# Performance work log

Measured on AMD Instinct MI355X. Metric: run time of the kernel, lower is better.

Reference implementation:

```python
import jax, jax.numpy as jnp
import numpy as np

B, N, D, A, R, E = 4, 50000, 128, 128, 200, 600000  # batch, entities, hidden dim, attn dim, relations, edges


def setup_inputs() -> dict:
    key = jax.random.key(0)
    ks = jax.random.split(key, 18)
    sD = 1.0 / np.sqrt(D)
    sA = 1.0 / np.sqrt(A)
    id_bat = jax.random.randint(ks[0], (E,), 0, B)
    id_sub = id_bat * N + jax.random.randint(ks[1], (E,), 0, N)
    id_rel = jax.random.randint(ks[2], (E,), 0, R)
    id_obj = id_bat * N + jax.random.randint(ks[3], (E,), 0, N)
    edges = jnp.stack([id_bat, id_sub, id_rel, id_obj], axis=1)
    return {
        "query": jax.random.normal(ks[4], (B, D), jnp.float32),
        "q_sub": jax.random.randint(ks[5], (B,), 0, N),
        "q_rel": jax.random.randint(ks[6], (B,), 0, R),
        "hidden": jax.random.normal(ks[7], (B, N, D), jnp.float32),
        "edges": edges,
        "nodes": jax.random.randint(ks[8], (B, 2), 0, N),
        "Ws_attn_w": jax.random.normal(ks[9], (A, D), jnp.float32) * sD,
        "Wr_attn_w": jax.random.normal(ks[10], (A, D), jnp.float32) * sD,
        "Wqr_attn_w": jax.random.normal(ks[11], (A, D), jnp.float32) * sD,
        "Wqr_attn_b": jax.random.normal(ks[12], (A,), jnp.float32) * sD,
        "W_attn_w": jax.random.normal(ks[13], (1, A), jnp.float32) * sA,
        "rela_embed": jax.random.normal(ks[14], (R, D), jnp.float32) * sD,
        "mlp1_w": jax.random.normal(ks[15], (D, D), jnp.float32) * sD,
        "mlp1_b": jnp.zeros((D,), jnp.float32),
        "mlp2_w": jax.random.normal(ks[16], (D, D), jnp.float32) * sD,
        "mlp2_b": jnp.zeros((D,), jnp.float32),
    }


def reference(query, q_sub, q_rel, hidden, edges, nodes,
              Ws_attn_w, Wr_attn_w, Wqr_attn_w, Wqr_attn_b, W_attn_w,
              rela_embed, mlp1_w, mlp1_b, mlp2_w, mlp2_b):
    b, n, d = hidden.shape
    id_bat, id_sub, id_rel, id_obj = edges[:, 0], edges[:, 1], edges[:, 2], edges[:, 3]
    all_ent = hidden.reshape(b * n, d)                       # [B*N, D]
    mh = all_ent[id_sub]                                     # [E, D] gather heads
    mr = rela_embed[id_rel]                                  # [E, D] gather relations
    mq = query[id_bat]                                       # [E, D] gather queries
    mess = mh * mr                                           # distmult message
    # attention MLP: sigmoid(W_attn @ relu(Ws h + Wr r + Wqr q + b))
    h_attn = jax.nn.relu(mh @ Ws_attn_w.T + mr @ Wr_attn_w.T + mq @ Wqr_attn_w.T + Wqr_attn_b)
    alpha = jax.nn.sigmoid(h_attn @ W_attn_w.T)              # [E, 1]
    message = mess * alpha
    # scatter-sum aggregate over destination nodes
    agg = jax.ops.segment_sum(message, id_obj, num_segments=b * n)   # [B*N, D]
    # mask of nodes that received at least one message (== torch.unique(id_obj))
    deg = jax.ops.segment_sum(jnp.ones((id_obj.shape[0],), jnp.float32), id_obj, num_segments=b * n)
    recv = deg > 0                                           # [B*N]
    # per-row MLP: Linear -> Linear -> ReLU (mlp_num=2, no activation between)
    h = jax.nn.relu((agg @ mlp1_w.T + mlp1_b) @ mlp2_w.T + mlp2_b)
    new_hidden = jnp.where(recv[:, None], h, 0.0).reshape(b, n, d)
    return new_hidden
```

## Files before the change

### kernel.cpp

```cpp
#include <hip/hip_runtime.h>

typedef unsigned int u32;
typedef unsigned short u16;
typedef __attribute__((ext_vector_type(8))) short bf16x8;
typedef __attribute__((ext_vector_type(4))) float f32x4;

#define Bb 4
#define Nn 50000
#define Dd 128
#define Rr 200
#define BN (Bb*Nn)
#define MAXDEG 32
#define LDW 136

__device__ __forceinline__ float bfs(u16 u) { return __uint_as_float(((u32)u) << 16); }
__device__ __forceinline__ float bflo(u32 u) { return __uint_as_float(u << 16); }
__device__ __forceinline__ float bfhi(u32 u) { return __uint_as_float(u & 0xffff0000u); }
__device__ __forceinline__ u16 f2bf(float f) {
    u32 x = __float_as_uint(f);
    return (u16)((x + 0x7fffu + ((x >> 16) & 1u)) >> 16);
}
template<bool BF>
__device__ __forceinline__ float ld1(const void* p, int i) {
    if (BF) return bfs(((const u16*)p)[i]);
    else    return ((const float*)p)[i];
}

__global__ void k_probe(const u32* __restrict__ q, int* __restrict__ flag) {
    int t = threadIdx.x;
    u32 w = q[t];
    int e = (int)((w >> 7) & 0xffu);
    bool plaus = (e >= 100 && e <= 150);
    unsigned long long m = __ballot(plaus);
    if (t == 0) flag[0] = (__popcll(m) >= 56) ? 1 : 0;
}

__global__ __launch_bounds__(256) void k_wprep(
    const void* Ws, const void* w1, const void* w2,
    const void* b1, const void* b2, const void* wattn, const void* rela,
    u16* WsH, u16* WsL, u16* w1H, u16* w1L, u16* w2H, u16* w2L,
    float* b1f, float* b2f, float* wattnf, float* relaf, const int* flag) {
    bool bf = (*flag != 0);
    int i = blockIdx.x * 256 + threadIdx.x;
    if (i < 16384) {
        float x = bf ? bfs(((const u16*)Ws)[i]) : ((const float*)Ws)[i];
        u16 h = f2bf(x); WsH[i] = h; WsL[i] = f2bf(x - bfs(h));
    } else if (i < 32768) {
        int j = i - 16384;
        float x = bf ? bfs(((const u16*)w1)[j]) : ((const float*)w1)[j];
        u16 h = f2bf(x); w1H[j] = h; w1L[j] = f2bf(x - bfs(h));
    } else if (i < 49152) {
        int j = i - 32768;
        float x = bf ? bfs(((const u16*)w2)[j]) : ((const float*)w2)[j];
        u16 h = f2bf(x); w2H[j] = h; w2L[j] = f2bf(x - bfs(h));
    } else if (i < 49152 + 128) {
        int j = i - 49152;
        b1f[j] = bf ? bfs(((const u16*)b1)[j]) : ((const float*)b1)[j];
    } else if (i < 49152 + 256) {
        int j = i - 49152 - 128;
        b2f[j] = bf ? bfs(((const u16*)b2)[j]) : ((const float*)b2)[j];
    } else if (i < 49152 + 384) {
        int j = i - 49152 - 256;
        wattnf[j] = bf ? bfs(((const u16*)wattn)[j]) : ((const float*)wattn)[j];
    } else if (i < 49152 + 384 + 25600) {
        int j = i - 49152 - 384;
        relaf[j] = bf ? bfs(((const u16*)rela)[j]) : ((const float*)rela)[j];
    }
}

template<bool BF>
__device__ __forceinline__ float dotrow1(const void* W, int row, const float* s) {
    float acc = 0.f;
    if (BF) {
        const uint4* wv = (const uint4*)((const u16*)W + row * Dd);
#pragma unroll
        for (int k = 0; k < 16; k++) {
            uint4 u = wv[k];
            acc += bflo(u.x)*s[k*8+0] + bfhi(u.x)*s[k*8+1]
                 + bflo(u.y)*s[k*8+2] + bfhi(u.y)*s[k*8+3]
                 + bflo(u.z)*s[k*8+4] + bfhi(u.z)*s[k*8+5]
                 + bflo(u.w)*s[k*8+6] + bfhi(u.w)*s[k*8+7];
        }
    } else {
        const float4* wv = (const float4*)((const float*)W + row * Dd);
#pragma unroll
        for (int k = 0; k < 32; k++) {
            float4 u = wv[k];
            acc += u.x*s[4*k] + u.y*s[4*k+1] + u.z*s[4*k+2] + u.w*s[4*k+3];
        }
    }
    return acc;
}
template<bool BF>
__device__ void k_wrq_body(const void* Wr, const void* Wqr, const void* bias,
                           const void* rela, const void* query, float* wrq) {
    int br = blockIdx.x;
    int b = br / Rr, r = br % Rr;
    int a = threadIdx.x;
    __shared__ float s[2 * Dd];
    s[a]      = ld1<BF>(rela,  r * Dd + a);
    s[Dd + a] = ld1<BF>(query, b * Dd + a);
    __syncthreads();
    wrq[br * Dd + a] = ld1<BF>(bias, a) + dotrow1<BF>(Wr, a, s) + dotrow1<BF>(Wqr, a, s + Dd);
}
__global__ __launch_bounds__(128) void k_wrq(const void* Wr, const void* Wqr, const void* bias,
                                             const void* rela, const void* query, float* wrq,
                                             const int* flag) {
    if (*flag) k_wrq_body<true>(Wr, Wqr, bias, rela, query, wrq);
    else       k_wrq_body<false>(Wr, Wqr, bias, rela, query, wrq);
}

__device__ __forceinline__ void stage_f32(const float* src, u16* Ah, u16* Al, int t) {
#pragma unroll
    for (int it = 0; it < 8; it++) {
        int idx = it * 256 + t;
        int row = idx >> 5, c4 = (idx & 31) << 2;
        float4 v = ((const float4*)src)[idx];
        u16 h0 = f2bf(v.x), h1 = f2bf(v.y), h2 = f2bf(v.z), h3 = f2bf(v.w);
        ushort4 hv; hv.x = h0; hv.y = h1; hv.z = h2; hv.w = h3;
        ushort4 lv; lv.x = f2bf(v.x - bfs(h0)); lv.y = f2bf(v.y - bfs(h1));
                    lv.z = f2bf(v.z - bfs(h2)); lv.w = f2bf(v.w - bfs(h3));
        *(ushort4*)(Ah + row * LDW + c4) = hv;
        *(ushort4*)(Al + row * LDW + c4) = lv;
    }
}
__device__ __forceinline__ void stage_bf(const u16* src, u16* Ah, u16* Al, int t) {
#pragma unroll
    for (int it = 0; it < 4; it++) {
        int idx = it * 256 + t;
        int row = idx >> 4, c8 = (idx & 15) << 3;
        uint4 v = ((const uint4*)src)[idx];
        *(uint4*)(Ah + row * LDW + c8) = v;
        uint4 z; z.x = 0; z.y = 0; z.z = 0; z.w = 0;
        *(uint4*)(Al + row * LDW + c8) = z;
    }
}

template<bool BF>
__device__ void k_hs_body(const void* hidden, const u16* WsH, const u16* WsL, u16* hs) {
    __shared__ u16 Ah[64 * LDW], Al[64 * LDW];
    int t = threadIdx.x, n0 = blockIdx.x * 64;
    if (BF) stage_bf((const u16*)hidden + (size_t)n0 * Dd, Ah, Al, t);
    else    stage_f32((const float*)hidden + (size_t)n0 * Dd, Ah, Al, t);
    __syncthreads();
    int w = t >> 6, lane = t & 63, m16 = lane & 15, quad = lane >> 4;
    const u16* rowh = Ah + (w * 16 + m16) * LDW + quad * 8;
    const u16* rowl = Al + (w * 16 + m16) * LDW + quad * 8;
    bf16x8 ah[4], al[4];
#pragma unroll
    for (int ks = 0; ks < 4; ks++) {
        ah[ks] = *(const bf16x8*)(rowh + ks * 32);
        al[ks] = *(const bf16x8*)(rowl + ks * 32);
    }
#pragma unroll
    for (int nt = 0; nt < 8; nt++) {
        int n = nt * 16 + m16;
        f32x4 acc = {0.f, 0.f, 0.f, 0.f};
#pragma unroll
        for (int ks = 0; ks < 4; ks++) {
            bf16x8 bh = *(const bf16x8*)(WsH + n * Dd + ks * 32 + quad * 8);
            bf16x8 bl = *(const bf16x8*)(WsL + n * Dd + ks * 32 + quad * 8);
            acc = __builtin_amdgcn_mfma_f32_16x16x32_bf16(ah[ks], bh, acc, 0, 0, 0);
            acc = __builtin_amdgcn_mfma_f32_16x16x32_bf16(al[ks], bh, acc, 0, 0, 0);
            acc = __builtin_amdgcn_mfma_f32_16x16x32_bf16(ah[ks], bl, acc, 0, 0, 0);
        }
#pragma unroll
        for (int r = 0; r < 4; r++) {
            int node = n0 + w * 16 + quad * 4 + r;
            hs[(size_t)node * Dd + n] = f2bf(acc[r]);
        }
    }
}
__global__ __launch_bounds__(256) void k_hs(const void* hidden, const u16* WsH, const u16* WsL,
                                            u16* hs, const int* flag) {
    if (*flag) k_hs_body<true>(hidden, WsH, WsL, hs);
    else       k_hs_body<false>(hidden, WsH, WsL, hs);
}

__global__ __launch_bounds__(256) void k_scatter(const int* __restrict__ edges,
                                                 u32* __restrict__ slots, u32* __restrict__ eslot,
                                                 int* __restrict__ deg, int nE) {
    int i = blockIdx.x * 256 + threadIdx.x;
    if (i >= nE) return;
    int bat = edges[4*i], sub = edges[4*i+1], rel = edges[4*i+2], obj = edges[4*i+3];
    int pos = atomicAdd(&deg[obj], 1);
    if (pos < MAXDEG) {
        u32 sl = (u32)obj * MAXDEG + pos;
        slots[sl] = (u32)sub | ((u32)rel << 18) | ((u32)bat << 26);
        eslot[i] = sl;
    } else eslot[i] = 0xFFFFFFFFu;
}

__global__ __launch_bounds__(256) void k_alpha(const int4* __restrict__ edges,
                                               const u16* __restrict__ hs,
                                               const float* __restrict__ wrq,
                                               const float* __restrict__ wattnf,
                                               const u32* __restrict__ eslot,
                                               float* __restrict__ alphaslot, int nE) {
    int wid = ((blockIdx.x * 256) + threadIdx.x) >> 6;
    int lane = threadIdx.x & 63;
    if (wid >= nE) return;
    int4 e = edges[wid];
    int bat = e.x, sub = e.y, rel = e.z;
    u32 hp = ((const u32*)hs)[sub * 64 + lane];
    float2 wq = ((const float2*)wrq)[(bat * Rr + rel) * 64 + lane];
    float2 wa = ((const float2*)wattnf)[lane];
    float h0 = fmaxf(bflo(hp) + wq.x, 0.f);
    float h1 = fmaxf(bfhi(hp) + wq.y, 0.f);
    float p = h0 * wa.x + h1 * wa.y;
#pragma unroll
    for (int m = 32; m >= 1; m >>= 1) p += __shfl_xor(p, m);
    if (lane == 0) {
        u32 sl = eslot[wid];
        if (sl != 0xFFFFFFFFu) alphaslot[sl] = 1.f / (1.f + __expf(-p));
    }
}

template<bool BF>
__device__ void k_agg_body(const u32* __restrict__ slots, const float* __restrict__ alphaslot,
                           const int* __restrict__ deg, const void* __restrict__ hidden,
                           const float* __restrict__ relaf, float* __restrict__ agg) {
    int wid = ((blockIdx.x * 256) + threadIdx.x) >> 6;
    int lane = threadIdx.x & 63;
    if (wid >= BN) return;
    int d = deg[wid]; if (d > MAXDEG) d = MAXDEG;
    float a0 = 0.f, a1 = 0.f;
    for (int e = 0; e < d; e++) {
        u32 rec = slots[wid * MAXDEG + e];
        float alpha = alphaslot[wid * MAXDEG + e];
        int sub = rec & 0x3FFFF, rel = (rec >> 18) & 0xFF;
        float mh0, mh1;
        if (BF) { u32 mh = ((const u32*)hidden)[sub * 64 + lane]; mh0 = bflo(mh); mh1 = bfhi(mh); }
        else    { float2 mh = ((const float2*)hidden)[sub * 64 + lane]; mh0 = mh.x; mh1 = mh.y; }
        float2 mr = ((const float2*)relaf)[rel * 64 + lane];
        a0 += mh0 * mr.x * alpha;
        a1 += mh1 * mr.y * alpha;
    }
    float2 v; v.x = a0; v.y = a1;
    ((float2*)agg)[(size_t)wid * 64 + lane] = v;
}
__global__ __launch_bounds__(256) void k_agg(const u32* slots, const float* alphaslot,
                                             const int* deg, const void* hidden,
                                             const float* relaf, float* agg, const int* flag) {
    if (*flag) k_agg_body<true>(slots, alphaslot, deg, hidden, relaf, agg);
    else       k_agg_body<false>(slots, alphaslot, deg, hidden, relaf, agg);
}

template<bool BF>
__device__ void k_mlp_body(const float* agg, const int* deg,
                           const u16* w1H, const u16* w1L, const u16* w2H, const u16* w2L,
                           const float* b1f, const float* b2f, void* out) {
    __shared__ u16 Ah[64 * LDW], Al[64 * LDW];
    int t = threadIdx.x, n0 = blockIdx.x * 64;
    stage_f32(agg + (size_t)n0 * Dd, Ah, Al, t);
    __syncthreads();
    int w = t >> 6, lane = t & 63, m16 = lane & 15, quad = lane >> 4;
    u16* rowh = Ah + (w * 16 + m16) * LDW + quad * 8;
    u16* rowl = Al + (w * 16 + m16) * LDW + quad * 8;
    bf16x8 ah[4], al[4];
#pragma unroll
    for (int ks = 0; ks < 4; ks++) {
        ah[ks] = *(const bf16x8*)(rowh + ks * 32);
        al[ks] = *(const bf16x8*)(rowl + ks * 32);
    }
#pragma unroll
    for (int nt = 0; nt < 8; nt++) {
        int n = nt * 16 + m16;
        f32x4 acc = {0.f, 0.f, 0.f, 0.f};
#pragma unroll
        for (int ks = 0; ks < 4; ks++) {
            bf16x8 bh = *(const bf16x8*)(w1H + n * Dd + ks * 32 + quad * 8);
            bf16x8 bl = *(const bf16x8*)(w1L + n * Dd + ks * 32 + quad * 8);
            acc = __builtin_amdgcn_mfma_f32_16x16x32_bf16(ah[ks], bh, acc, 0, 0, 0);
            acc = __builtin_amdgcn_mfma_f32_16x16x32_bf16(al[ks], bh, acc, 0, 0, 0);
            acc = __builtin_amdgcn_mfma_f32_16x16x32_bf16(ah[ks], bl, acc, 0, 0, 0);
        }
        float bv = b1f[n];
#pragma unroll
        for (int r = 0; r < 4; r++) {
            float v = acc[r] + bv;
            int row = w * 16 + quad * 4 + r;
            u16 h = f2bf(v);
            Ah[row * LDW + n] = h;
            Al[row * LDW + n] = f2bf(v - bfs(h));
        }
    }
    bf16x8 mh[4], ml[4];
#pragma unroll
    for (int ks = 0; ks < 4; ks++) {
        mh[ks] = *(const bf16x8*)(rowh + ks * 32);
        ml[ks] = *(const bf16x8*)(rowl + ks * 32);
    }
    int dg[4];
#pragma unroll
    for (int r = 0; r < 4; r++) dg[r] = deg[n0 + w * 16 + quad * 4 + r];
#pragma unroll
    for (int nt = 0; nt < 8; nt++) {
        int n = nt * 16 + m16;
        f32x4 acc = {0.f, 0.f, 0.f, 0.f};
#pragma unroll
        for (int ks = 0; ks < 4; ks++) {
            bf16x8 bh = *(const bf16x8*)(w2H + n * Dd + ks * 32 + quad * 8);
            bf16x8 bl = *(const bf16x8*)(w2L + n * Dd + ks * 32 + quad * 8);
            acc = __builtin_amdgcn_mfma_f32_16x16x32_bf16(mh[ks], bh, acc, 0, 0, 0);
            acc = __builtin_amdgcn_mfma_f32_16x16x32_bf16(ml[ks], bh, acc, 0, 0, 0);
            acc = __builtin_amdgcn_mfma_f32_16x16x32_bf16(mh[ks], bl, acc, 0, 0, 0);
        }
        float bv = b2f[n];
#pragma unroll
        for (int r = 0; r < 4; r++) {
            float v = fmaxf(acc[r] + bv, 0.f);
            if (dg[r] == 0) v = 0.f;
            size_t o = (size_t)(n0 + w * 16 + quad * 4 + r) * Dd + n;
            if (BF) ((u16*)out)[o] = f2bf(v);
            else    ((float*)out)[o] = v;
        }
    }
}
__global__ __launch_bounds__(256) void k_mlp(const float* agg, const int* deg,
                                             const u16* w1H, const u16* w1L,
                                             const u16* w2H, const u16* w2L,
                                             const float* b1f, const float* b2f,
                                             void* out, const int* flag) {
    if (*flag) k_mlp_body<true>(agg, deg, w1H, w1L, w2H, w2L, b1f, b2f, out);
    else       k_mlp_body<false>(agg, deg, w1H, w1L, w2H, w2L, b1f, b2f, out);
}

extern "C" void kernel_launch(void* const* d_in, const int* in_sizes, int n_in,
                              void* d_out, int out_size, void* d_ws, size_t ws_size,
                              hipStream_t stream) {
    const void* query  = d_in[0];
    const void* hidden = d_in[3];
    const int*  edges  = (const int*)d_in[4];
    const void* Ws     = d_in[6];
    const void* Wr     = d_in[7];
    const void* Wqr    = d_in[8];
    const void* Wqrb   = d_in[9];
    const void* Wattn  = d_in[10];
    const void* rela   = d_in[11];
    const void* w1     = d_in[12];
    const void* b1     = d_in[13];
    const void* w2     = d_in[14];
    const void* b2     = d_in[15];

    char* ws = (char*)d_ws;
    float* agg    = (float*)ws;
    u16*   hs     = (u16*)ws;
    float* wrq    = (float*)(ws +  51200000);
    u32*   eslot  = (u32*) (ws +  51609600);
    u32*   slots  = (u32*) (ws + 102400000);
    float* alphas = (float*)(ws + 128000000);
    int*   deg    = (int*) (ws + 153600000);
    u16*   WsH    = (u16*) (ws + 154400000);
    u16*   WsL    = (u16*) (ws + 154432768);
    u16*   w1H    = (u16*) (ws + 154465536);
    u16*   w1L    = (u16*) (ws + 154498304);
    u16*   w2H    = (u16*) (ws + 154531072);
    u16*   w2L    = (u16*) (ws + 154563840);
    float* b1f    = (float*)(ws + 154596608);
    float* b2f    = (float*)(ws + 154597120);
    float* wattnf = (float*)(ws + 154597632);
    float* relaf  = (float*)(ws + 154598144);
    int*   flag   = (int*) (ws + 154700544);

    int nE = in_sizes[4] / 4;

    k_probe<<<1, 64, 0, stream>>>((const u32*)query, flag);
    hipMemsetAsync(deg, 0, (size_t)BN * 4, stream);
    k_wprep<<<294, 256, 0, stream>>>(Ws, w1, w2, b1, b2, Wattn, rela,
                                     WsH, WsL, w1H, w1L, w2H, w2L,
                                     b1f, b2f, wattnf, relaf, flag);
    k_wrq<<<Bb * Rr, 128, 0, stream>>>(Wr, Wqr, Wqrb, rela, query, wrq, flag);
    k_hs<<<BN / 64, 256, 0, stream>>>(hidden, WsH, WsL, hs, flag);
    k_scatter<<<(nE + 255) / 256, 256, 0, stream>>>(edges, slots, eslot, deg, nE);
    k_alpha<<<(nE + 3) / 4, 256, 0, stream>>>((const int4*)edges, hs, wrq, wattnf,
                                              eslot, alphas, nE);
    k_agg<<<(BN + 3) / 4, 256, 0, stream>>>(slots, alphas, deg, hidden, relaf, agg, flag);
    k_mlp<<<BN / 64, 256, 0, stream>>>(agg, deg, w1H, w1L, w2H, w2L, b1f, b2f, d_out, flag);
}
```

Measured before the change: 826.7 us.

## Fuse alpha, aggregation and MLP into one per-wave kernel

```diff
diff --git a/kernel.cpp b/kernel.cpp
--- a/kernel.cpp
+++ b/kernel.cpp
@@ -12,6 +12,7 @@
 #define BN (Bb*Nn)
 #define MAXDEG 32
 #define LDW 136
+#define SLAB 4352
 
 __device__ __forceinline__ float bfs(u16 u) { return __uint_as_float(((u32)u) << 16); }
 __device__ __forceinline__ float bflo(u32 u) { return __uint_as_float(u << 16); }
@@ -110,47 +111,46 @@
     else       k_wrq_body<false>(Wr, Wqr, bias, rela, query, wrq);
 }
 
-__device__ __forceinline__ void stage_f32(const float* src, u16* Ah, u16* Al, int t) {
-#pragma unroll
-    for (int it = 0; it < 8; it++) {
-        int idx = it * 256 + t;
-        int row = idx >> 5, c4 = (idx & 31) << 2;
-        float4 v = ((const float4*)src)[idx];
-        u16 h0 = f2bf(v.x), h1 = f2bf(v.y), h2 = f2bf(v.z), h3 = f2bf(v.w);
-        ushort4 hv; hv.x = h0; hv.y = h1; hv.z = h2; hv.w = h3;
-        ushort4 lv; lv.x = f2bf(v.x - bfs(h0)); lv.y = f2bf(v.y - bfs(h1));
-                    lv.z = f2bf(v.z - bfs(h2)); lv.w = f2bf(v.w - bfs(h3));
-        *(ushort4*)(Ah + row * LDW + c4) = hv;
-        *(ushort4*)(Al + row * LDW + c4) = lv;
-    }
-}
-__device__ __forceinline__ void stage_bf(const u16* src, u16* Ah, u16* Al, int t) {
-#pragma unroll
-    for (int it = 0; it < 4; it++) {
-        int idx = it * 256 + t;
-        int row = idx >> 4, c8 = (idx & 15) << 3;
-        uint4 v = ((const uint4*)src)[idx];
-        *(uint4*)(Ah + row * LDW + c8) = v;
-        uint4 z; z.x = 0; z.y = 0; z.z = 0; z.w = 0;
-        *(uint4*)(Al + row * LDW + c8) = z;
-    }
-}
-
-template<bool BF>
-__device__ void k_hs_body(const void* hidden, const u16* WsH, const u16* WsL, u16* hs) {
-    __shared__ u16 Ah[64 * LDW], Al[64 * LDW];
-    int t = threadIdx.x, n0 = blockIdx.x * 64;
-    if (BF) stage_bf((const u16*)hidden + (size_t)n0 * Dd, Ah, Al, t);
-    else    stage_f32((const float*)hidden + (size_t)n0 * Dd, Ah, Al, t);
-    __syncthreads();
-    int w = t >> 6, lane = t & 63, m16 = lane & 15, quad = lane >> 4;
-    const u16* rowh = Ah + (w * 16 + m16) * LDW + quad * 8;
-    const u16* rowl = Al + (w * 16 + m16) * LDW + quad * 8;
+template<bool BF>
+__device__ void hs_body(const void* hidden, const u16* WsH, const u16* WsL, u16* hs) {
+    __shared__ u16 SL[4][SLAB];
+    int t = threadIdx.x, w = t >> 6, lane = t & 63;
+    int m16 = lane & 15, quad = lane >> 4;
+    int base = blockIdx.x * 64 + w * 16;
+    u16* Smh = SL[w];
+    u16* Sml = SL[w] + 16 * LDW;
+
+    if (BF) {
+        const u16* src = (const u16*)hidden + (size_t)base * Dd;
+#pragma unroll
+        for (int j = 0; j < 4; j++) {
+            int flat = j * 64 + lane;
+            int row = flat >> 4, c8 = (flat & 15) * 8;
+            uint4 v = ((const uint4*)src)[flat];
+            *(uint4*)(Smh + row * LDW + c8) = v;
+        }
+    } else {
+        const float* src = (const float*)hidden + (size_t)base * Dd;
+#pragma unroll
+        for (int j = 0; j < 8; j++) {
+            int flat = j * 64 + lane;
+            int row = flat >> 5, c4 = (flat & 31) * 4;
+            float4 v = ((const float4*)src)[flat];
+            u16 h0 = f2bf(v.x), h1 = f2bf(v.y), h2 = f2bf(v.z), h3 = f2bf(v.w);
+            ushort4 hv; hv.x = h0; hv.y = h1; hv.z = h2; hv.w = h3;
+            ushort4 lv; lv.x = f2bf(v.x - bfs(h0)); lv.y = f2bf(v.y - bfs(h1));
+                        lv.z = f2bf(v.z - bfs(h2)); lv.w = f2bf(v.w - bfs(h3));
+            *(ushort4*)(Smh + row * LDW + c4) = hv;
+            *(ushort4*)(Sml + row * LDW + c4) = lv;
+        }
+    }
+    const u16* ph = Smh + m16 * LDW + quad * 8;
+    const u16* pl = Sml + m16 * LDW + quad * 8;
     bf16x8 ah[4], al[4];
 #pragma unroll
     for (int ks = 0; ks < 4; ks++) {
-        ah[ks] = *(const bf16x8*)(rowh + ks * 32);
-        al[ks] = *(const bf16x8*)(rowl + ks * 32);
+        ah[ks] = *(const bf16x8*)(ph + ks * 32);
+        if (!BF) al[ks] = *(const bf16x8*)(pl + ks * 32);
     }
 #pragma unroll
     for (int nt = 0; nt < 8; nt++) {
@@ -159,109 +159,102 @@
 #pragma unroll
         for (int ks = 0; ks < 4; ks++) {
             bf16x8 bh = *(const bf16x8*)(WsH + n * Dd + ks * 32 + quad * 8);
-            bf16x8 bl = *(const bf16x8*)(WsL + n * Dd + ks * 32 + quad * 8);
             acc = __builtin_amdgcn_mfma_f32_16x16x32_bf16(ah[ks], bh, acc, 0, 0, 0);
-            acc = __builtin_amdgcn_mfma_f32_16x16x32_bf16(al[ks], bh, acc, 0, 0, 0);
-            acc = __builtin_amdgcn_mfma_f32_16x16x32_bf16(ah[ks], bl, acc, 0, 0, 0);
-        }
-#pragma unroll
-        for (int r = 0; r < 4; r++) {
-            int node = n0 + w * 16 + quad * 4 + r;
-            hs[(size_t)node * Dd + n] = f2bf(acc[r]);
-        }
-    }
-}
-__global__ __launch_bounds__(256) void k_hs(const void* hidden, const u16* WsH, const u16* WsL,
-                                            u16* hs, const int* flag) {
-    if (*flag) k_hs_body<true>(hidden, WsH, WsL, hs);
-    else       k_hs_body<false>(hidden, WsH, WsL, hs);
+            if (!BF) {
+                bf16x8 bl = *(const bf16x8*)(WsL + n * Dd + ks * 32 + quad * 8);
+                acc = __builtin_amdgcn_mfma_f32_16x16x32_bf16(al[ks], bh, acc, 0, 0, 0);
+                acc = __builtin_amdgcn_mfma_f32_16x16x32_bf16(ah[ks], bl, acc, 0, 0, 0);
+            }
+        }
+#pragma unroll
+        for (int r = 0; r < 4; r++)
+            hs[(size_t)(base + quad * 4 + r) * Dd + n] = f2bf(acc[r]);
+    }
+}
+__global__ __launch_bounds__(256, 4) void k_hs(const void* hidden, const u16* WsH,
+                                               const u16* WsL, u16* hs, const int* flag) {
+    if (*flag) hs_body<true>(hidden, WsH, WsL, hs);
+    else       hs_body<false>(hidden, WsH, WsL, hs);
 }
 
 __global__ __launch_bounds__(256) void k_scatter(const int* __restrict__ edges,
-                                                 u32* __restrict__ slots, u32* __restrict__ eslot,
+                                                 u32* __restrict__ slots,
                                                  int* __restrict__ deg, int nE) {
     int i = blockIdx.x * 256 + threadIdx.x;
     if (i >= nE) return;
     int bat = edges[4*i], sub = edges[4*i+1], rel = edges[4*i+2], obj = edges[4*i+3];
     int pos = atomicAdd(&deg[obj], 1);
-    if (pos < MAXDEG) {
-        u32 sl = (u32)obj * MAXDEG + pos;
-        slots[sl] = (u32)sub | ((u32)rel << 18) | ((u32)bat << 26);
-        eslot[i] = sl;
-    } else eslot[i] = 0xFFFFFFFFu;
-}
-
-__global__ __launch_bounds__(256) void k_alpha(const int4* __restrict__ edges,
-                                               const u16* __restrict__ hs,
-                                               const float* __restrict__ wrq,
-                                               const float* __restrict__ wattnf,
-                                               const u32* __restrict__ eslot,
-                                               float* __restrict__ alphaslot, int nE) {
-    int wid = ((blockIdx.x * 256) + threadIdx.x) >> 6;
-    int lane = threadIdx.x & 63;
-    if (wid >= nE) return;
-    int4 e = edges[wid];
-    int bat = e.x, sub = e.y, rel = e.z;
+    if (pos < MAXDEG)
+        slots[obj * MAXDEG + pos] = (u32)sub | ((u32)rel << 18) | ((u32)bat << 26);
+}
+
+template<bool BF>
+__device__ __forceinline__ void edge_msg(u32 rec, int lane, float2 wa,
+                                         const u16* hs, const float* wrq,
+                                         const void* hidden, const float* relaf,
+                                         float& a0, float& a1) {
+    int sub = rec & 0x3FFFF, rel = (rec >> 18) & 0xFF, bat = (int)(rec >> 26);
     u32 hp = ((const u32*)hs)[sub * 64 + lane];
     float2 wq = ((const float2*)wrq)[(bat * Rr + rel) * 64 + lane];
-    float2 wa = ((const float2*)wattnf)[lane];
+    float mh0, mh1;
+    if (BF) { u32 mh = ((const u32*)hidden)[sub * 64 + lane]; mh0 = bflo(mh); mh1 = bfhi(mh); }
+    else    { float2 mh = ((const float2*)hidden)[sub * 64 + lane]; mh0 = mh.x; mh1 = mh.y; }
+    float2 mr = ((const float2*)relaf)[rel * 64 + lane];
     float h0 = fmaxf(bflo(hp) + wq.x, 0.f);
     float h1 = fmaxf(bfhi(hp) + wq.y, 0.f);
     float p = h0 * wa.x + h1 * wa.y;
 #pragma unroll
     for (int m = 32; m >= 1; m >>= 1) p += __shfl_xor(p, m);
-    if (lane == 0) {
-        u32 sl = eslot[wid];
-        if (sl != 0xFFFFFFFFu) alphaslot[sl] = 1.f / (1.f + __expf(-p));
-    }
-}
-
-template<bool BF>
-__device__ void k_agg_body(const u32* __restrict__ slots, const float* __restrict__ alphaslot,
-                           const int* __restrict__ deg, const void* __restrict__ hidden,
-                           const float* __restrict__ relaf, float* __restrict__ agg) {
-    int wid = ((blockIdx.x * 256) + threadIdx.x) >> 6;
-    int lane = threadIdx.x & 63;
-    if (wid >= BN) return;
-    int d = deg[wid]; if (d > MAXDEG) d = MAXDEG;
-    float a0 = 0.f, a1 = 0.f;
-    for (int e = 0; e < d; e++) {
-        u32 rec = slots[wid * MAXDEG + e];
-        float alpha = alphaslot[wid * MAXDEG + e];
-        int sub = rec & 0x3FFFF, rel = (rec >> 18) & 0xFF;
-        float mh0, mh1;
-        if (BF) { u32 mh = ((const u32*)hidden)[sub * 64 + lane]; mh0 = bflo(mh); mh1 = bfhi(mh); }
-        else    { float2 mh = ((const float2*)hidden)[sub * 64 + lane]; mh0 = mh.x; mh1 = mh.y; }
-        float2 mr = ((const float2*)relaf)[rel * 64 + lane];
-        a0 += mh0 * mr.x * alpha;
-        a1 += mh1 * mr.y * alpha;
-    }
-    float2 v; v.x = a0; v.y = a1;
-    ((float2*)agg)[(size_t)wid * 64 + lane] = v;
-}
-__global__ __launch_bounds__(256) void k_agg(const u32* slots, const float* alphaslot,
-                                             const int* deg, const void* hidden,
-                                             const float* relaf, float* agg, const int* flag) {
-    if (*flag) k_agg_body<true>(slots, alphaslot, deg, hidden, relaf, agg);
-    else       k_agg_body<false>(slots, alphaslot, deg, hidden, relaf, agg);
-}
-
-template<bool BF>
-__device__ void k_mlp_body(const float* agg, const int* deg,
+    float alpha = 1.f / (1.f + __expf(-p));
+    a0 += mh0 * mr.x * alpha;
+    a1 += mh1 * mr.y * alpha;
+}
+
+template<bool BF>
+__device__ void fused_body(const u32* __restrict__ slots, const int* __restrict__ deg,
+                           const u16* __restrict__ hs, const float* __restrict__ wrq,
+                           const float* __restrict__ wattnf,
+                           const void* __restrict__ hidden, const float* __restrict__ relaf,
                            const u16* w1H, const u16* w1L, const u16* w2H, const u16* w2L,
                            const float* b1f, const float* b2f, void* out) {
-    __shared__ u16 Ah[64 * LDW], Al[64 * LDW];
-    int t = threadIdx.x, n0 = blockIdx.x * 64;
-    stage_f32(agg + (size_t)n0 * Dd, Ah, Al, t);
-    __syncthreads();
-    int w = t >> 6, lane = t & 63, m16 = lane & 15, quad = lane >> 4;
-    u16* rowh = Ah + (w * 16 + m16) * LDW + quad * 8;
-    u16* rowl = Al + (w * 16 + m16) * LDW + quad * 8;
+    __shared__ u16 SL[4][SLAB];
+    int t = threadIdx.x, w = t >> 6, lane = t & 63;
+    int m16 = lane & 15, quad = lane >> 4;
+    int base = blockIdx.x * 64 + w * 16;
+    u16* Smh = SL[w];
+    u16* Sml = SL[w] + 16 * LDW;
+    float2 wa = ((const float2*)wattnf)[lane];
+
+    for (int i = 0; i < 16; i++) {
+        int node = base + i;
+        int d = deg[node]; if (d > MAXDEG) d = MAXDEG;
+        float a0 = 0.f, a1 = 0.f;
+        float c0 = 0.f, c1 = 0.f;
+        int e = 0;
+        for (; e + 1 < d; e += 2) {
+            u32 r0 = slots[node * MAXDEG + e];
+            u32 r1 = slots[node * MAXDEG + e + 1];
+            edge_msg<BF>(r0, lane, wa, hs, wrq, hidden, relaf, a0, a1);
+            edge_msg<BF>(r1, lane, wa, hs, wrq, hidden, relaf, c0, c1);
+        }
+        if (e < d) {
+            u32 r0 = slots[node * MAXDEG + e];
+            edge_msg<BF>(r0, lane, wa, hs, wrq, hidden, relaf, a0, a1);
+        }
+        a0 += c0; a1 += c1;
+        u16 h0 = f2bf(a0); u16 l0 = f2bf(a0 - bfs(h0));
+        u16 h1 = f2bf(a1); u16 l1 = f2bf(a1 - bfs(h1));
+        *(u32*)(Smh + i * LDW + 2 * lane) = (u32)h0 | ((u32)h1 << 16);
+        *(u32*)(Sml + i * LDW + 2 * lane) = (u32)l0 | ((u32)l1 << 16);
+    }
+
+    const u16* ph = Smh + m16 * LDW + quad * 8;
+    const u16* pl = Sml + m16 * LDW + quad * 8;
     bf16x8 ah[4], al[4];
 #pragma unroll
     for (int ks = 0; ks < 4; ks++) {
-        ah[ks] = *(const bf16x8*)(rowh + ks * 32);
-        al[ks] = *(const bf16x8*)(rowl + ks * 32);
+        ah[ks] = *(const bf16x8*)(ph + ks * 32);
+        al[ks] = *(const bf16x8*)(pl + ks * 32);
     }
 #pragma unroll
     for (int nt = 0; nt < 8; nt++) {
@@ -270,30 +263,33 @@
 #pragma unroll
         for (int ks = 0; ks < 4; ks++) {
             bf16x8 bh = *(const bf16x8*)(w1H + n * Dd + ks * 32 + quad * 8);
-            bf16x8 bl = *(const bf16x8*)(w1L + n * Dd + ks * 32 + quad * 8);
             acc = __builtin_amdgcn_mfma_f32_16x16x32_bf16(ah[ks], bh, acc, 0, 0, 0);
             acc = __builtin_amdgcn_mfma_f32_16x16x32_bf16(al[ks], bh, acc, 0, 0, 0);
-            acc = __builtin_amdgcn_mfma_f32_16x16x32_bf16(ah[ks], bl, acc, 0, 0, 0);
+            if (!BF) {
+                bf16x8 bl = *(const bf16x8*)(w1L + n * Dd + ks * 32 + quad * 8);
+                acc = __builtin_amdgcn_mfma_f32_16x16x32_bf16(ah[ks], bl, acc, 0, 0, 0);
+            }
         }
         float bv = b1f[n];
 #pragma unroll
         for (int r = 0; r < 4; r++) {
             float v = acc[r] + bv;
-            int row = w * 16 + quad * 4 + r;
+            int row = quad * 4 + r;
             u16 h = f2bf(v);
-            Ah[row * LDW + n] = h;
-            Al[row * LDW + n] = f2bf(v - bfs(h));
-        }
-    }
+            Smh[row * LDW + n] = h;
+            Sml[row * LDW + n] = f2bf(v - bfs(h));
+        }
+    }
+
     bf16x8 mh[4], ml[4];
 #pragma unroll
     for (int ks = 0; ks < 4; ks++) {
-        mh[ks] = *(const bf16x8*)(rowh + ks * 32);
-        ml[ks] = *(const bf16x8*)(rowl + ks * 32);
+        mh[ks] = *(const bf16x8*)(ph + ks * 32);
+        ml[ks] = *(const bf16x8*)(pl + ks * 32);
     }
     int dg[4];
 #pragma unroll
-    for (int r = 0; r < 4; r++) dg[r] = deg[n0 + w * 16 + quad * 4 + r];
+    for (int r = 0; r < 4; r++) dg[r] = deg[base + quad * 4 + r];
 #pragma unroll
     for (int nt = 0; nt < 8; nt++) {
         int n = nt * 16 + m16;
@@ -301,29 +297,36 @@
 #pragma unroll
         for (int ks = 0; ks < 4; ks++) {
             bf16x8 bh = *(const bf16x8*)(w2H + n * Dd + ks * 32 + quad * 8);
-            bf16x8 bl = *(const bf16x8*)(w2L + n * Dd + ks * 32 + quad * 8);
             acc = __builtin_amdgcn_mfma_f32_16x16x32_bf16(mh[ks], bh, acc, 0, 0, 0);
             acc = __builtin_amdgcn_mfma_f32_16x16x32_bf16(ml[ks], bh, acc, 0, 0, 0);
-            acc = __builtin_amdgcn_mfma_f32_16x16x32_bf16(mh[ks], bl, acc, 0, 0, 0);
+            if (!BF) {
+                bf16x8 bl = *(const bf16x8*)(w2L + n * Dd + ks * 32 + quad * 8);
+                acc = __builtin_amdgcn_mfma_f32_16x16x32_bf16(mh[ks], bl, acc, 0, 0, 0);
+            }
         }
         float bv = b2f[n];
 #pragma unroll
         for (int r = 0; r < 4; r++) {
             float v = fmaxf(acc[r] + bv, 0.f);
             if (dg[r] == 0) v = 0.f;
-            size_t o = (size_t)(n0 + w * 16 + quad * 4 + r) * Dd + n;
+            size_t o = (size_t)(base + quad * 4 + r) * Dd + n;
             if (BF) ((u16*)out)[o] = f2bf(v);
             else    ((float*)out)[o] = v;
         }
     }
 }
-__global__ __launch_bounds__(256) void k_mlp(const float* agg, const int* deg,
-                                             const u16* w1H, const u16* w1L,
-                                             const u16* w2H, const u16* w2L,
-                                             const float* b1f, const float* b2f,
-                                             void* out, const int* flag) {
-    if (*flag) k_mlp_body<true>(agg, deg, w1H, w1L, w2H, w2L, b1f, b2f, out);
-    else       k_mlp_body<false>(agg, deg, w1H, w1L, w2H, w2L, b1f, b2f, out);
+__global__ __launch_bounds__(256, 4) void k_fused(const u32* slots, const int* deg,
+                                                  const u16* hs, const float* wrq,
+                                                  const float* wattnf, const void* hidden,
+                                                  const float* relaf,
+                                                  const u16* w1H, const u16* w1L,
+                                                  const u16* w2H, const u16* w2L,
+                                                  const float* b1f, const float* b2f,
+                                                  void* out, const int* flag) {
+    if (*flag) fused_body<true>(slots, deg, hs, wrq, wattnf, hidden, relaf,
+                                w1H, w1L, w2H, w2L, b1f, b2f, out);
+    else       fused_body<false>(slots, deg, hs, wrq, wattnf, hidden, relaf,
+                                 w1H, w1L, w2H, w2L, b1f, b2f, out);
 }
 
 extern "C" void kernel_launch(void* const* d_in, const int* in_sizes, int n_in,
@@ -344,24 +347,21 @@
     const void* b2     = d_in[15];
 
     char* ws = (char*)d_ws;
-    float* agg    = (float*)ws;
     u16*   hs     = (u16*)ws;
     float* wrq    = (float*)(ws +  51200000);
-    u32*   eslot  = (u32*) (ws +  51609600);
-    u32*   slots  = (u32*) (ws + 102400000);
-    float* alphas = (float*)(ws + 128000000);
-    int*   deg    = (int*) (ws + 153600000);
-    u16*   WsH    = (u16*) (ws + 154400000);
-    u16*   WsL    = (u16*) (ws + 154432768);
-    u16*   w1H    = (u16*) (ws + 154465536);
-    u16*   w1L    = (u16*) (ws + 154498304);
-    u16*   w2H    = (u16*) (ws + 154531072);
-    u16*   w2L    = (u16*) (ws + 154563840);
-    float* b1f    = (float*)(ws + 154596608);
-    float* b2f    = (float*)(ws + 154597120);
-    float* wattnf = (float*)(ws + 154597632);
-    float* relaf  = (float*)(ws + 154598144);
-    int*   flag   = (int*) (ws + 154700544);
+    u32*   slots  = (u32*) (ws +  51609600);
+    int*   deg    = (int*) (ws +  77209600);
+    u16*   WsH    = (u16*) (ws +  78009600);
+    u16*   WsL    = (u16*) (ws +  78042368);
+    u16*   w1H    = (u16*) (ws +  78075136);
+    u16*   w1L    = (u16*) (ws +  78107904);
+    u16*   w2H    = (u16*) (ws +  78140672);
+    u16*   w2L    = (u16*) (ws +  78173440);
+    float* b1f    = (float*)(ws +  78206208);
+    float* b2f    = (float*)(ws +  78206720);
+    float* wattnf = (float*)(ws +  78207232);
+    float* relaf  = (float*)(ws +  78207744);
+    int*   flag   = (int*) (ws +  78310144);
 
     int nE = in_sizes[4] / 4;
 
@@ -372,9 +372,7 @@
                                      b1f, b2f, wattnf, relaf, flag);
     k_wrq<<<Bb * Rr, 128, 0, stream>>>(Wr, Wqr, Wqrb, rela, query, wrq, flag);
     k_hs<<<BN / 64, 256, 0, stream>>>(hidden, WsH, WsL, hs, flag);
-    k_scatter<<<(nE + 255) / 256, 256, 0, stream>>>(edges, slots, eslot, deg, nE);
-    k_alpha<<<(nE + 3) / 4, 256, 0, stream>>>((const int4*)edges, hs, wrq, wattnf,
-                                              eslot, alphas, nE);
-    k_agg<<<(BN + 3) / 4, 256, 0, stream>>>(slots, alphas, deg, hidden, relaf, agg, flag);
-    k_mlp<<<BN / 64, 256, 0, stream>>>(agg, deg, w1H, w1L, w2H, w2L, b1f, b2f, d_out, flag);
-}
+    k_scatter<<<(nE + 255) / 256, 256, 0, stream>>>(edges, slots, deg, nE);
+    k_fused<<<BN / 64, 256, 0, stream>>>(slots, deg, hs, wrq, wattnf, hidden, relaf,
+                                         w1H, w1L, w2H, w2L, b1f, b2f, d_out, flag);
+}
```

Result: faster. 788.9 us (-4.6%).
